# Optimization experiments

Measured on AMD Instinct MI355X. Metric: run time of the kernel, lower is better.

Reference implementation:

```python
import jax, jax.numpy as jnp
import numpy as np

N_NODES = 50000
N_EDGES = 800000
SIZES = [128, 256, 256, 128]
EPS = 1e-5


def setup_inputs() -> dict:
    key = jax.random.key(0)
    ks = jax.random.split(key, 2 + 5 * (len(SIZES) - 1))
    inp = {
        "x": jax.random.normal(ks[0], (N_NODES, SIZES[0]), dtype=jnp.float32),
        "edge_index": jax.random.randint(ks[1], (2, N_EDGES), 0, N_NODES, dtype=jnp.int64),
    }
    k = 2
    for i, (fin, fout) in enumerate(zip(SIZES[:-1], SIZES[1:])):
        scale = 1.0 / np.sqrt(fin)
        inp[f"W{i}"] = jax.random.normal(ks[k], (fout, fin), dtype=jnp.float32) * scale; k += 1
        inp[f"b{i}"] = jnp.zeros((fout,), dtype=jnp.float32)
        inp[f"g{i}"] = jnp.ones((fout,), dtype=jnp.float32)   # LayerNorm weight
        inp[f"be{i}"] = jnp.zeros((fout,), dtype=jnp.float32)  # LayerNorm bias
        inp[f"a{i}"] = jnp.full((1,), 0.25, dtype=jnp.float32)  # PReLU slope
        k += 3  # keep key consumption deterministic
    return inp


def _gcn_conv(x, src, dst, dinv, W, b):
    # GCNConv: h = x @ W^T; aggregate norm(src,dst) * h[src] into dst; add bias.
    h = x @ W.T  # [N, F_out]
    norm = dinv[src] * dinv[dst]  # [E+N]
    msg = norm[:, None] * h[src]  # [E+N, F_out]
    return jax.ops.segment_sum(msg, dst, num_segments=N_NODES) + b


def _layernorm_graph(x, g, be):
    # PyG LayerNorm(mode='graph'): normalize over all nodes and channels.
    mu = x.mean()
    xc = x - mu
    var = (xc * xc).mean()
    return xc / jnp.sqrt(var + EPS) * g + be


def _prelu(x, a):
    return jnp.where(x >= 0, x, a * x)


def reference(x, edge_index, W0, b0, g0, be0, a0, W1, b1, g1, be1, a1, W2, b2, g2, be2, a2):
    loop = jnp.arange(N_NODES, dtype=edge_index.dtype)
    src = jnp.concatenate([edge_index[0], loop])  # add self-loops
    dst = jnp.concatenate([edge_index[1], loop])
    deg = jax.ops.segment_sum(jnp.ones_like(dst, dtype=x.dtype), dst, num_segments=N_NODES)
    dinv = jax.lax.rsqrt(deg)  # deg >= 1 due to self-loops
    params = [(W0, b0, g0, be0, a0), (W1, b1, g1, be1, a1), (W2, b2, g2, be2, a2)]
    for W, b, g, be, a in params:
        x = _gcn_conv(x, src, dst, dinv, W, b)
        x = _layernorm_graph(x, g, be)
        x = _prelu(x, a)
    return x
```

## Files before the change

kernel.cpp:

```cpp
#include <hip/hip_runtime.h>

#define N_NODES 50000
#define N_EDGES 800000
#define EPS 1e-5f

typedef __attribute__((ext_vector_type(8))) short bf16x8;
typedef __attribute__((ext_vector_type(4))) float f32x4;
typedef __attribute__((ext_vector_type(4))) unsigned short us4;

__device__ __forceinline__ unsigned short f2b(float f) {
    union { float f; unsigned int u; } v; v.f = f;
    unsigned int r = v.u + 0x7fffu + ((v.u >> 16) & 1u);
    return (unsigned short)(r >> 16);
}
__device__ __forceinline__ float b2f(unsigned short b) {
    union { unsigned int u; float f; } v; v.u = ((unsigned int)b) << 16;
    return v.f;
}

#define RED_BUCKETS 64
#define RED_FLOATS_PER_LAYER (RED_BUCKETS * 16)


__global__ void init_kernel(int* __restrict__ deg, int* __restrict__ fill,
                            float* __restrict__ red, int n) {
    int i = blockIdx.x * blockDim.x + threadIdx.x;
    if (i < n) { deg[i] = 0; fill[i] = 0; }
    if (i < 3 * RED_FLOATS_PER_LAYER) red[i] = 0.f;
}

__global__ void count_kernel(const int* __restrict__ dst, int* __restrict__ deg, int e) {
    for (int i = blockIdx.x * blockDim.x + threadIdx.x; i < e; i += gridDim.x * blockDim.x)
        atomicAdd(&deg[dst[i]], 1);
}

__global__ void scan1_kernel(const int* __restrict__ deg, float* __restrict__ dinv,
                             int* __restrict__ bsum, int n) {
    int i = blockIdx.x * 256 + threadIdx.x;
    int v = (i < n) ? deg[i] : 0;
    if (i < n) dinv[i] = rsqrtf((float)(v + 1));
    int t = v;
    #pragma unroll
    for (int off = 1; off < 64; off <<= 1) t += __shfl_xor(t, off);
    __shared__ int wsum[4];
    int wid = threadIdx.x >> 6, lane = threadIdx.x & 63;
    if (lane == 0) wsum[wid] = t;
    __syncthreads();
    if (threadIdx.x == 0) bsum[blockIdx.x] = wsum[0] + wsum[1] + wsum[2] + wsum[3];
}

__global__ void scan2_kernel(const int* __restrict__ bsum, int* __restrict__ bpre, int nb) {
    __shared__ int sm[256];
    int t = threadIdx.x;
    sm[t] = (t < nb) ? bsum[t] : 0;
    __syncthreads();
    #pragma unroll
    for (int d = 1; d < 256; d <<= 1) {
        int x = (t >= d) ? sm[t - d] : 0;
        __syncthreads();
        sm[t] += x;
        __syncthreads();
    }
    bpre[t] = (t > 0) ? sm[t - 1] : 0;
}

__global__ void scan3_kernel(const int* __restrict__ deg, const int* __restrict__ bpre,
                             int* __restrict__ off, int n) {
    __shared__ int sm[256];
    int t = threadIdx.x;
    int i = blockIdx.x * 256 + t;
    int v = (i < n) ? deg[i] : 0;
    sm[t] = v;
    __syncthreads();
    #pragma unroll
    for (int d = 1; d < 256; d <<= 1) {
        int x = (t >= d) ? sm[t - d] : 0;
        __syncthreads();
        sm[t] += x;
        __syncthreads();
    }
    if (i < n) off[i + 1] = sm[t] + bpre[blockIdx.x];
    if (i == 0) off[0] = 0;
}

__global__ void scatter_kernel(const int* __restrict__ src, const int* __restrict__ dst,
                               const int* __restrict__ coff, int* __restrict__ fill,
                               const float* __restrict__ dinv,
                               int2* __restrict__ epack, int e) {
    for (int i = blockIdx.x * blockDim.x + threadIdx.x; i < e; i += gridDim.x * blockDim.x) {
        int d = dst[i];
        int s = src[i];
        int pos = coff[d] + atomicAdd(&fill[d], 1);
        epack[pos] = make_int2(s, __float_as_int(dinv[s] * dinv[d]));
    }
}


#define CV_NX (N_NODES * 128 / 4)
#define CV_N0 (256 * 128 / 4)
#define CV_N1 (256 * 256 / 4)
#define CV_N2 (128 * 256 / 4)

__global__ void convert_all(const float* __restrict__ x0, const float* __restrict__ W0,
                            const float* __restrict__ W1, const float* __restrict__ W2,
                            unsigned short* __restrict__ xb, unsigned short* __restrict__ wb0,
                            unsigned short* __restrict__ wb1, unsigned short* __restrict__ wb2) {
    int i = blockIdx.x * 256 + threadIdx.x;
    const float* s;
    unsigned short* d;
    int j = i;
    if (j < CV_NX) { s = x0; d = xb; }
    else if ((j -= CV_NX) < CV_N0) { s = W0; d = wb0; }
    else if ((j -= CV_N0) < CV_N1) { s = W1; d = wb1; }
    else if ((j -= CV_N1) < CV_N2) { s = W2; d = wb2; }
    else return;
    float4 v = reinterpret_cast<const float4*>(s)[j];
    us4 o;
    o[0] = f2b(v.x); o[1] = f2b(v.y); o[2] = f2b(v.z); o[3] = f2b(v.w);
    reinterpret_cast<us4*>(d)[j] = o;
}


template<int BN, bool TRANSFORM, bool ADD_BIAS, bool FUSE_RED>
__global__ __launch_bounds__(256) void gemm_fused(
    const unsigned short* __restrict__ Xin, const unsigned short* __restrict__ Wb,
    const float* __restrict__ bias, const float* __restrict__ redin,
    const float* __restrict__ gw, const float* __restrict__ bw,
    const float* __restrict__ asl, float* __restrict__ redout,
    unsigned short* __restrict__ Hout, int M, int K, float inv_count) {
    constexpr int FR_N = BN / 64;
    __shared__ unsigned short xs[64 * 32];
    __shared__ unsigned short wsm[BN * 32];
    int m0 = blockIdx.x * 64;
    int tid = threadIdx.x;
    int wid = tid >> 6, lane = tid & 63;
    int l16 = lane & 15, kg = lane >> 4;
    int srow = tid >> 2, sblk = tid & 3;

    float mu = 0.f, rstd = 0.f, alpha = 0.f;
    if (TRANSFORM) {
        float s = redin[lane * 16], s2 = redin[lane * 16 + 1];
        #pragma unroll
        for (int off = 1; off < 64; off <<= 1) { s += __shfl_xor(s, off); s2 += __shfl_xor(s2, off); }
        mu = s * inv_count;
        rstd = rsqrtf(s2 * inv_count - mu * mu + EPS);
        alpha = asl[0];
    }

    f32x4 acc[4][FR_N] = {};
    for (int k0 = 0; k0 < K; k0 += 32) {
        int gm = m0 + srow;
        bf16x8 xv = {};
        if (gm < M) {
            bf16x8 u = *reinterpret_cast<const bf16x8*>(Xin + (size_t)gm * K + k0 + sblk * 8);
            if (TRANSFORM) {
                #pragma unroll
                for (int i = 0; i < 8; ++i) {
                    int f = k0 + sblk * 8 + i;
                    float v = (b2f((unsigned short)u[i]) - mu) * rstd * gw[f] + bw[f];
                    v = v >= 0.f ? v : alpha * v;
                    xv[i] = (short)f2b(v);
                }
            } else {
                xv = u;
            }
        }
        *reinterpret_cast<bf16x8*>(xs + srow * 32 + ((sblk ^ (srow & 3)) * 8)) = xv;
        #pragma unroll
        for (int i = 0; i < BN / 64; ++i) {
            int idx = tid + i * 256;
            int wrow = idx >> 2, wblk = idx & 3;
            bf16x8 wv = *reinterpret_cast<const bf16x8*>(Wb + (size_t)wrow * K + k0 + wblk * 8);
            *reinterpret_cast<bf16x8*>(wsm + wrow * 32 + ((wblk ^ (wrow & 3)) * 8)) = wv;
        }
        __syncthreads();
        bf16x8 a[4], b[FR_N];
        #pragma unroll
        for (int f = 0; f < 4; ++f) {
            int ar = f * 16 + l16;
            a[f] = *reinterpret_cast<const bf16x8*>(xs + ar * 32 + ((kg ^ (ar & 3)) * 8));
        }
        #pragma unroll
        for (int f = 0; f < FR_N; ++f) {
            int br = wid * (FR_N * 16) + f * 16 + l16;
            b[f] = *reinterpret_cast<const bf16x8*>(wsm + br * 32 + ((kg ^ (br & 3)) * 8));
        }
        #pragma unroll
        for (int i = 0; i < 4; ++i)
            #pragma unroll
            for (int j = 0; j < FR_N; ++j)
                acc[i][j] = __builtin_amdgcn_mfma_f32_16x16x32_bf16(a[i], b[j], acc[i][j], 0, 0, 0);
        __syncthreads();
    }

    float s = 0.f, s2 = 0.f;
    #pragma unroll
    for (int i = 0; i < 4; ++i) {
        #pragma unroll
        for (int j = 0; j < FR_N; ++j) {
            int col = wid * (FR_N * 16) + j * 16 + l16;
            float bv = ADD_BIAS ? bias[col] : 0.f;
            #pragma unroll
            for (int r = 0; r < 4; ++r) {
                int row = m0 + i * 16 + kg * 4 + r;
                if (row < M) {
                    float v = acc[i][j][r] + bv;
                    if (FUSE_RED) { s += v; s2 += v * v; }
                    Hout[(size_t)row * BN + col] = f2b(v);
                }
            }
        }
    }
    if (FUSE_RED) {
        #pragma unroll
        for (int off = 1; off < 64; off <<= 1) { s += __shfl_xor(s, off); s2 += __shfl_xor(s2, off); }
        if (lane == 0) {
            int bkt = (blockIdx.x & (RED_BUCKETS - 1)) * 16;
            atomicAdd(&redout[bkt], s);
            atomicAdd(&redout[bkt + 1], s2);
        }
    }
}


template<int COLS, bool ADD_BIAS, bool FUSE_RED>
__global__ void aggregate2(const unsigned short* __restrict__ Hb,
                           const int* __restrict__ coff, const int2* __restrict__ epack,
                           const float* __restrict__ dinv,
                           const float* __restrict__ bias, unsigned short* __restrict__ Y,
                           float* __restrict__ red) {
    constexpr int RL = COLS / 8;
    constexpr int NG = 64 / RL;
    int node = blockIdx.x * 4 + (threadIdx.x >> 6);
    int lane = threadIdx.x & 63;
    int g = lane / RL;
    int rl = lane % RL;
    float di = dinv[node];
    int s0 = coff[node], s1 = coff[node + 1];
    float acc[8] = {};

    int k = s0 - 1 + g;
    int2 ec;
    bf16x8 vc;
    bool have = (k < s1);
    if (have) {
        if (k < s0) ec = make_int2(node, __float_as_int(di * di));
        else ec = epack[k];
        vc = *reinterpret_cast<const bf16x8*>(Hb + (size_t)ec.x * COLS + rl * 8);
    }
    while (have) {
        int k2 = k + NG;
        bool have2 = (k2 < s1);
        int2 en;
        bf16x8 vn;
        if (have2) {
            en = epack[k2];
            vn = *reinterpret_cast<const bf16x8*>(Hb + (size_t)en.x * COLS + rl * 8);
        }
        float w = __int_as_float(ec.y);
        #pragma unroll
        for (int i = 0; i < 8; ++i) acc[i] += w * b2f((unsigned short)vc[i]);
        k = k2; ec = en; vc = vn; have = have2;
    }

    #pragma unroll
    for (int off = RL; off < 64; off <<= 1) {
        #pragma unroll
        for (int i = 0; i < 8; ++i) acc[i] += __shfl_xor(acc[i], off);
    }
    if (ADD_BIAS) {
        #pragma unroll
        for (int i = 0; i < 8; ++i) acc[i] += bias[rl * 8 + i];
    }
    if (FUSE_RED) {
        float s = 0.f, s2 = 0.f;
        if (g == 0) {
            #pragma unroll
            for (int i = 0; i < 8; ++i) { s += acc[i]; s2 += acc[i] * acc[i]; }
        }
        #pragma unroll
        for (int off = 1; off < 64; off <<= 1) { s += __shfl_xor(s, off); s2 += __shfl_xor(s2, off); }
        if (lane == 0) {
            int bkt = (blockIdx.x & (RED_BUCKETS - 1)) * 16;
            atomicAdd(&red[bkt], s);
            atomicAdd(&red[bkt + 1], s2);
        }
    }
    if (g == 0) {
        bf16x8 o;
        #pragma unroll
        for (int i = 0; i < 8; ++i) o[i] = (short)f2b(acc[i]);
        __builtin_nontemporal_store(o, reinterpret_cast<bf16x8*>(Y + (size_t)node * COLS + rl * 8));
    }
}


__global__ void norm_final(const unsigned short* __restrict__ Yb, const float* __restrict__ red,
                           const float* __restrict__ g, const float* __restrict__ be,
                           const float* __restrict__ a, float* __restrict__ X,
                           int fmask8, int n8, float inv_count) {
    int lane = threadIdx.x & 63;
    float s = red[lane * 16], s2 = red[lane * 16 + 1];
    #pragma unroll
    for (int off = 1; off < 64; off <<= 1) { s += __shfl_xor(s, off); s2 += __shfl_xor(s2, off); }
    float mu = s * inv_count;
    float rstd = rsqrtf(s2 * inv_count - mu * mu + EPS);
    float alpha = a[0];
    for (int i = blockIdx.x * blockDim.x + threadIdx.x; i < n8; i += gridDim.x * blockDim.x) {
        bf16x8 v = reinterpret_cast<const bf16x8*>(Yb)[i];
        int fb = (i & fmask8) * 8;
        float o[8];
        #pragma unroll
        for (int j = 0; j < 8; ++j) {
            float t = (b2f((unsigned short)v[j]) - mu) * rstd * g[fb + j] + be[fb + j];
            o[j] = t >= 0.f ? t : alpha * t;
        }
        float* xp = X + (size_t)i * 8;
        *reinterpret_cast<float4*>(xp) = make_float4(o[0], o[1], o[2], o[3]);
        *reinterpret_cast<float4*>(xp + 4) = make_float4(o[4], o[5], o[6], o[7]);
    }
}


extern "C" void kernel_launch(void* const* d_in, const int* in_sizes, int n_in,
                              void* d_out, int out_size, void* d_ws, size_t ws_size,
                              hipStream_t stream) {
    const float* x0 = (const float*)d_in[0];
    const int* ei = (const int*)d_in[1];
    const float* W[3] = {(const float*)d_in[2], (const float*)d_in[7], (const float*)d_in[12]};
    const float* bb[3] = {(const float*)d_in[3], (const float*)d_in[8], (const float*)d_in[13]};
    const float* gg[3] = {(const float*)d_in[4], (const float*)d_in[9], (const float*)d_in[14]};
    const float* be[3] = {(const float*)d_in[5], (const float*)d_in[10], (const float*)d_in[15]};
    const float* aa[3] = {(const float*)d_in[6], (const float*)d_in[11], (const float*)d_in[16]};

    char* ws = (char*)d_ws;
    size_t o = 0;
    auto alloc = [&](size_t bytes) {
        void* p = ws + o;
        o = (o + bytes + 255) & ~(size_t)255;
        return p;
    };
    int* deg = (int*)alloc(N_NODES * 4);
    int* fill = (int*)alloc(N_NODES * 4);
    int* coff = (int*)alloc((N_NODES + 1) * 4);
    int2* epack = (int2*)alloc((size_t)N_EDGES * 8);
    float* dinv = (float*)alloc(N_NODES * 4);
    int* bsum = (int*)alloc(256 * 4);
    int* bpre = (int*)alloc(256 * 4);
    float* red = (float*)alloc(3 * RED_FLOATS_PER_LAYER * 4);
    unsigned short* Wb0 = (unsigned short*)alloc(256 * 128 * 2);
    unsigned short* Wb1 = (unsigned short*)alloc(256 * 256 * 2);
    unsigned short* Wb2 = (unsigned short*)alloc(128 * 256 * 2);
    unsigned short* xb = (unsigned short*)alloc((size_t)N_NODES * 128 * 2);
    unsigned short* hb = (unsigned short*)alloc((size_t)N_NODES * 256 * 2);
    unsigned short* yb = (unsigned short*)alloc((size_t)N_NODES * 256 * 2);

    const int* e_src = ei;
    const int* e_dst = ei + N_EDGES;
    int nb = (N_NODES + 255) / 256;

    init_kernel<<<(N_NODES + 255) / 256, 256, 0, stream>>>(deg, fill, red, N_NODES);
    count_kernel<<<2048, 256, 0, stream>>>(e_dst, deg, N_EDGES);
    scan1_kernel<<<nb, 256, 0, stream>>>(deg, dinv, bsum, N_NODES);
    scan2_kernel<<<1, 256, 0, stream>>>(bsum, bpre, nb);
    scan3_kernel<<<nb, 256, 0, stream>>>(deg, bpre, coff, N_NODES);
    scatter_kernel<<<2048, 256, 0, stream>>>(e_src, e_dst, coff, fill, dinv, epack, N_EDGES);

    int cvtot = CV_NX + CV_N0 + CV_N1 + CV_N2;
    convert_all<<<(cvtot + 255) / 256, 256, 0, stream>>>(x0, W[0], W[1], W[2], xb, Wb0, Wb1, Wb2);

    int gm = (N_NODES + 63) / 64;

    aggregate2<128, false, false><<<12500, 256, 0, stream>>>(xb, coff, epack, dinv,
                                                             nullptr, hb, nullptr);
    gemm_fused<256, false, true, true><<<gm, 256, 0, stream>>>(
        hb, Wb0, bb[0], nullptr, nullptr, nullptr, nullptr, red + 0, yb, N_NODES, 128,
        1.0f / (N_NODES * 256.0f));

    gemm_fused<256, true, false, false><<<gm, 256, 0, stream>>>(
        yb, Wb1, nullptr, red + 0, gg[0], be[0], aa[0], nullptr, hb, N_NODES, 256,
        1.0f / (N_NODES * 256.0f));
    aggregate2<256, true, true><<<12500, 256, 0, stream>>>(
        hb, coff, epack, dinv, bb[1], yb, red + RED_FLOATS_PER_LAYER);

    gemm_fused<128, true, false, false><<<gm, 256, 0, stream>>>(
        yb, Wb2, nullptr, red + RED_FLOATS_PER_LAYER, gg[1], be[1], aa[1], nullptr, hb,
        N_NODES, 256, 1.0f / (N_NODES * 256.0f));
    aggregate2<128, true, true><<<12500, 256, 0, stream>>>(
        hb, coff, epack, dinv, bb[2], yb, red + 2 * RED_FLOATS_PER_LAYER);

    norm_final<<<2048, 256, 0, stream>>>(yb, red + 2 * RED_FLOATS_PER_LAYER, gg[2], be[2], aa[2],
                                         (float*)d_out, 15, N_NODES * 128 / 8,
                                         1.0f / (N_NODES * 128.0f));
}
```

Measured before the change: 341.2 us.

## Pack edges into 32-bit words, double-buffer GEMM, and fold init into conversion

Each CSR edge is now one 32-bit word: a 16-bit source index plus a bf16 normalisation weight, where it used to be an int2. This halves edge traffic in the three aggregation passes. The GEMM stages only the activation tile in double-buffered LDS and reads weight fragments straight from global memory. It swaps the MFMA operand order so outputs go out as vectorised 4-element row stores, and folds LayerNorm/PReLU into fused fma form with vector loads of gamma/beta. Counter and reduction zeroing is merged into the conversion kernel to drop one launch. The risks are the bf16 precision loss on edge weights and a 16-bit index that only holds while there are fewer than 65536 nodes.

```diff
diff --git a/kernel.cpp b/kernel.cpp
--- a/kernel.cpp
+++ b/kernel.cpp
@@ -22,90 +22,20 @@
 #define RED_FLOATS_PER_LAYER (RED_BUCKETS * 16)
 
 
-__global__ void init_kernel(int* __restrict__ deg, int* __restrict__ fill,
-                            float* __restrict__ red, int n) {
-    int i = blockIdx.x * blockDim.x + threadIdx.x;
-    if (i < n) { deg[i] = 0; fill[i] = 0; }
-    if (i < 3 * RED_FLOATS_PER_LAYER) red[i] = 0.f;
-}
-
-__global__ void count_kernel(const int* __restrict__ dst, int* __restrict__ deg, int e) {
-    for (int i = blockIdx.x * blockDim.x + threadIdx.x; i < e; i += gridDim.x * blockDim.x)
-        atomicAdd(&deg[dst[i]], 1);
-}
-
-__global__ void scan1_kernel(const int* __restrict__ deg, float* __restrict__ dinv,
-                             int* __restrict__ bsum, int n) {
-    int i = blockIdx.x * 256 + threadIdx.x;
-    int v = (i < n) ? deg[i] : 0;
-    if (i < n) dinv[i] = rsqrtf((float)(v + 1));
-    int t = v;
-    #pragma unroll
-    for (int off = 1; off < 64; off <<= 1) t += __shfl_xor(t, off);
-    __shared__ int wsum[4];
-    int wid = threadIdx.x >> 6, lane = threadIdx.x & 63;
-    if (lane == 0) wsum[wid] = t;
-    __syncthreads();
-    if (threadIdx.x == 0) bsum[blockIdx.x] = wsum[0] + wsum[1] + wsum[2] + wsum[3];
-}
-
-__global__ void scan2_kernel(const int* __restrict__ bsum, int* __restrict__ bpre, int nb) {
-    __shared__ int sm[256];
-    int t = threadIdx.x;
-    sm[t] = (t < nb) ? bsum[t] : 0;
-    __syncthreads();
-    #pragma unroll
-    for (int d = 1; d < 256; d <<= 1) {
-        int x = (t >= d) ? sm[t - d] : 0;
-        __syncthreads();
-        sm[t] += x;
-        __syncthreads();
-    }
-    bpre[t] = (t > 0) ? sm[t - 1] : 0;
-}
-
-__global__ void scan3_kernel(const int* __restrict__ deg, const int* __restrict__ bpre,
-                             int* __restrict__ off, int n) {
-    __shared__ int sm[256];
-    int t = threadIdx.x;
-    int i = blockIdx.x * 256 + t;
-    int v = (i < n) ? deg[i] : 0;
-    sm[t] = v;
-    __syncthreads();
-    #pragma unroll
-    for (int d = 1; d < 256; d <<= 1) {
-        int x = (t >= d) ? sm[t - d] : 0;
-        __syncthreads();
-        sm[t] += x;
-        __syncthreads();
-    }
-    if (i < n) off[i + 1] = sm[t] + bpre[blockIdx.x];
-    if (i == 0) off[0] = 0;
-}
-
-__global__ void scatter_kernel(const int* __restrict__ src, const int* __restrict__ dst,
-                               const int* __restrict__ coff, int* __restrict__ fill,
-                               const float* __restrict__ dinv,
-                               int2* __restrict__ epack, int e) {
-    for (int i = blockIdx.x * blockDim.x + threadIdx.x; i < e; i += gridDim.x * blockDim.x) {
-        int d = dst[i];
-        int s = src[i];
-        int pos = coff[d] + atomicAdd(&fill[d], 1);
-        epack[pos] = make_int2(s, __float_as_int(dinv[s] * dinv[d]));
-    }
-}
-
-
 #define CV_NX (N_NODES * 128 / 4)
 #define CV_N0 (256 * 128 / 4)
 #define CV_N1 (256 * 256 / 4)
 #define CV_N2 (128 * 256 / 4)
 
-__global__ void convert_all(const float* __restrict__ x0, const float* __restrict__ W0,
+__global__ void prep_kernel(const float* __restrict__ x0, const float* __restrict__ W0,
                             const float* __restrict__ W1, const float* __restrict__ W2,
                             unsigned short* __restrict__ xb, unsigned short* __restrict__ wb0,
-                            unsigned short* __restrict__ wb1, unsigned short* __restrict__ wb2) {
+                            unsigned short* __restrict__ wb1, unsigned short* __restrict__ wb2,
+                            int* __restrict__ deg, int* __restrict__ fill,
+                            float* __restrict__ red) {
     int i = blockIdx.x * 256 + threadIdx.x;
+    if (i < N_NODES) { deg[i] = 0; fill[i] = 0; }
+    if (i < 3 * RED_FLOATS_PER_LAYER) red[i] = 0.f;
     const float* s;
     unsigned short* d;
     int j = i;
@@ -121,21 +51,88 @@
 }
 
 
+__global__ void count_kernel(const int* __restrict__ dst, int* __restrict__ deg, int e) {
+    for (int i = blockIdx.x * blockDim.x + threadIdx.x; i < e; i += gridDim.x * blockDim.x)
+        atomicAdd(&deg[dst[i]], 1);
+}
+
+__global__ void scan1_kernel(const int* __restrict__ deg, float* __restrict__ dinv,
+                             int* __restrict__ bsum, int n) {
+    int i = blockIdx.x * 256 + threadIdx.x;
+    int v = (i < n) ? deg[i] : 0;
+    if (i < n) dinv[i] = rsqrtf((float)(v + 1));
+    int t = v;
+    #pragma unroll
+    for (int off = 1; off < 64; off <<= 1) t += __shfl_xor(t, off);
+    __shared__ int wsum[4];
+    int wid = threadIdx.x >> 6, lane = threadIdx.x & 63;
+    if (lane == 0) wsum[wid] = t;
+    __syncthreads();
+    if (threadIdx.x == 0) bsum[blockIdx.x] = wsum[0] + wsum[1] + wsum[2] + wsum[3];
+}
+
+__global__ void scan2_kernel(const int* __restrict__ bsum, int* __restrict__ bpre, int nb) {
+    __shared__ int sm[256];
+    int t = threadIdx.x;
+    sm[t] = (t < nb) ? bsum[t] : 0;
+    __syncthreads();
+    #pragma unroll
+    for (int d = 1; d < 256; d <<= 1) {
+        int x = (t >= d) ? sm[t - d] : 0;
+        __syncthreads();
+        sm[t] += x;
+        __syncthreads();
+    }
+    bpre[t] = (t > 0) ? sm[t - 1] : 0;
+}
+
+__global__ void scan3_kernel(const int* __restrict__ deg, const int* __restrict__ bpre,
+                             int* __restrict__ off, int n) {
+    __shared__ int sm[256];
+    int t = threadIdx.x;
+    int i = blockIdx.x * 256 + t;
+    int v = (i < n) ? deg[i] : 0;
+    sm[t] = v;
+    __syncthreads();
+    #pragma unroll
+    for (int d = 1; d < 256; d <<= 1) {
+        int x = (t >= d) ? sm[t - d] : 0;
+        __syncthreads();
+        sm[t] += x;
+        __syncthreads();
+    }
+    if (i < n) off[i + 1] = sm[t] + bpre[blockIdx.x];
+    if (i == 0) off[0] = 0;
+}
+
+__global__ void scatter_kernel(const int* __restrict__ src, const int* __restrict__ dst,
+                               const int* __restrict__ coff, int* __restrict__ fill,
+                               const float* __restrict__ dinv,
+                               unsigned int* __restrict__ epack, int e) {
+    for (int i = blockIdx.x * blockDim.x + threadIdx.x; i < e; i += gridDim.x * blockDim.x) {
+        int d = dst[i];
+        int s = src[i];
+        int pos = coff[d] + atomicAdd(&fill[d], 1);
+        epack[pos] = ((unsigned int)f2b(dinv[s] * dinv[d]) << 16) | (unsigned int)s;
+    }
+}
+
+
 template<int BN, bool TRANSFORM, bool ADD_BIAS, bool FUSE_RED>
-__global__ __launch_bounds__(256) void gemm_fused(
+__device__ __forceinline__ void gemm_body(
     const unsigned short* __restrict__ Xin, const unsigned short* __restrict__ Wb,
     const float* __restrict__ bias, const float* __restrict__ redin,
     const float* __restrict__ gw, const float* __restrict__ bw,
     const float* __restrict__ asl, float* __restrict__ redout,
     unsigned short* __restrict__ Hout, int M, int K, float inv_count) {
     constexpr int FR_N = BN / 64;
-    __shared__ unsigned short xs[64 * 32];
-    __shared__ unsigned short wsm[BN * 32];
-    int m0 = blockIdx.x * 64;
+    __shared__ unsigned short xs[2][64 * 32];
     int tid = threadIdx.x;
     int wid = tid >> 6, lane = tid & 63;
     int l16 = lane & 15, kg = lane >> 4;
     int srow = tid >> 2, sblk = tid & 3;
+    int m0 = blockIdx.x * 64;
+    int colbase = wid * (BN / 4);
 
     float mu = 0.f, rstd = 0.f, alpha = 0.f;
     if (TRANSFORM) {
@@ -147,67 +144,85 @@
         alpha = asl[0];
     }
 
-    f32x4 acc[4][FR_N] = {};
-    for (int k0 = 0; k0 < K; k0 += 32) {
-        int gm = m0 + srow;
+    int gm = m0 + srow;
+    bool inm = (gm < M);
+    const unsigned short* xrow = Xin + (size_t)gm * K + sblk * 8;
+    unsigned short* xdst = &xs[0][srow * 32 + ((sblk ^ (srow & 3)) * 8)];
+
+    auto stage = [&](int k0, int buf) {
         bf16x8 xv = {};
-        if (gm < M) {
-            bf16x8 u = *reinterpret_cast<const bf16x8*>(Xin + (size_t)gm * K + k0 + sblk * 8);
+        if (inm) {
+            bf16x8 u = *reinterpret_cast<const bf16x8*>(xrow + k0);
             if (TRANSFORM) {
+                int f0 = k0 + sblk * 8;
+                float ga[8], ba[8];
+                *reinterpret_cast<float4*>(&ga[0]) = *reinterpret_cast<const float4*>(gw + f0);
+                *reinterpret_cast<float4*>(&ga[4]) = *reinterpret_cast<const float4*>(gw + f0 + 4);
+                *reinterpret_cast<float4*>(&ba[0]) = *reinterpret_cast<const float4*>(bw + f0);
+                *reinterpret_cast<float4*>(&ba[4]) = *reinterpret_cast<const float4*>(bw + f0 + 4);
                 #pragma unroll
                 for (int i = 0; i < 8; ++i) {
-                    int f = k0 + sblk * 8 + i;
-                    float v = (b2f((unsigned short)u[i]) - mu) * rstd * gw[f] + bw[f];
-                    v = v >= 0.f ? v : alpha * v;
+                    float A = rstd * ga[i];
+                    float B = ba[i] - mu * A;
+                    float v = fmaf(b2f((unsigned short)u[i]), A, B);
+                    v = fmaf(fminf(v, 0.f), alpha - 1.0f, v);
                     xv[i] = (short)f2b(v);
                 }
             } else {
                 xv = u;
             }
         }
-        *reinterpret_cast<bf16x8*>(xs + srow * 32 + ((sblk ^ (srow & 3)) * 8)) = xv;
-        #pragma unroll
-        for (int i = 0; i < BN / 64; ++i) {
-            int idx = tid + i * 256;
-            int wrow = idx >> 2, wblk = idx & 3;
-            bf16x8 wv = *reinterpret_cast<const bf16x8*>(Wb + (size_t)wrow * K + k0 + wblk * 8);
-            *reinterpret_cast<bf16x8*>(wsm + wrow * 32 + ((wblk ^ (wrow & 3)) * 8)) = wv;
-        }
+        *reinterpret_cast<bf16x8*>(xdst + buf * (64 * 32)) = xv;
+    };
+
+    stage(0, 0);
+    f32x4 acc[4][FR_N] = {};
+    int nsteps = K / 32;
+    for (int s = 0; s < nsteps; ++s) {
         __syncthreads();
-        bf16x8 a[4], b[FR_N];
-        #pragma unroll
-        for (int f = 0; f < 4; ++f) {
-            int ar = f * 16 + l16;
-            a[f] = *reinterpret_cast<const bf16x8*>(xs + ar * 32 + ((kg ^ (ar & 3)) * 8));
-        }
-        #pragma unroll
-        for (int f = 0; f < FR_N; ++f) {
-            int br = wid * (FR_N * 16) + f * 16 + l16;
-            b[f] = *reinterpret_cast<const bf16x8*>(wsm + br * 32 + ((kg ^ (br & 3)) * 8));
+        int k0 = s * 32;
+        if (s + 1 < nsteps) stage(k0 + 32, (s + 1) & 1);
+        bf16x8 b[FR_N];
+        #pragma unroll
+        for (int j = 0; j < FR_N; ++j)
+            b[j] = *reinterpret_cast<const bf16x8*>(
+                Wb + (size_t)(colbase + j * 16 + l16) * K + k0 + kg * 8);
+        const unsigned short* xbuf = xs[s & 1];
+        bf16x8 a[4];
+        #pragma unroll
+        for (int i = 0; i < 4; ++i) {
+            int ar = i * 16 + l16;
+            a[i] = *reinterpret_cast<const bf16x8*>(xbuf + ar * 32 + ((kg ^ (ar & 3)) * 8));
         }
         #pragma unroll
         for (int i = 0; i < 4; ++i)
             #pragma unroll
             for (int j = 0; j < FR_N; ++j)
-                acc[i][j] = __builtin_amdgcn_mfma_f32_16x16x32_bf16(a[i], b[j], acc[i][j], 0, 0, 0);
-        __syncthreads();
-    }
-
+                acc[i][j] = __builtin_amdgcn_mfma_f32_16x16x32_bf16(b[j], a[i], acc[i][j], 0, 0, 0);
+    }
+
+    float bsel[FR_N][4];
+    if (ADD_BIAS) {
+        #pragma unroll
+        for (int j = 0; j < FR_N; ++j)
+            *reinterpret_cast<float4*>(bsel[j]) =
+                *reinterpret_cast<const float4*>(bias + colbase + j * 16 + kg * 4);
+    }
     float s = 0.f, s2 = 0.f;
     #pragma unroll
     for (int i = 0; i < 4; ++i) {
-        #pragma unroll
-        for (int j = 0; j < FR_N; ++j) {
-            int col = wid * (FR_N * 16) + j * 16 + l16;
-            float bv = ADD_BIAS ? bias[col] : 0.f;
+        int row = m0 + i * 16 + l16;
+        if (row < M) {
             #pragma unroll
-            for (int r = 0; r < 4; ++r) {
-                int row = m0 + i * 16 + kg * 4 + r;
-                if (row < M) {
-                    float v = acc[i][j][r] + bv;
+            for (int j = 0; j < FR_N; ++j) {
+                us4 o;
+                #pragma unroll
+                for (int r = 0; r < 4; ++r) {
+                    float v = acc[i][j][r] + (ADD_BIAS ? bsel[j][r] : 0.f);
                     if (FUSE_RED) { s += v; s2 += v * v; }
-                    Hout[(size_t)row * BN + col] = f2b(v);
+                    o[r] = f2b(v);
                 }
+                *reinterpret_cast<us4*>(Hout + (size_t)row * BN + colbase + j * 16 + kg * 4) = o;
             }
         }
     }
@@ -224,11 +239,11 @@
 
 
 template<int COLS, bool ADD_BIAS, bool FUSE_RED>
-__global__ void aggregate2(const unsigned short* __restrict__ Hb,
-                           const int* __restrict__ coff, const int2* __restrict__ epack,
-                           const float* __restrict__ dinv,
-                           const float* __restrict__ bias, unsigned short* __restrict__ Y,
-                           float* __restrict__ red) {
+__device__ __forceinline__ void agg_body(
+    const unsigned short* __restrict__ Hb, const int* __restrict__ coff,
+    const unsigned int* __restrict__ epack, const float* __restrict__ dinv,
+    const float* __restrict__ bias, unsigned short* __restrict__ Y,
+    float* __restrict__ red) {
     constexpr int RL = COLS / 8;
     constexpr int NG = 64 / RL;
     int node = blockIdx.x * 4 + (threadIdx.x >> 6);
@@ -240,27 +255,27 @@
     float acc[8] = {};
 
     int k = s0 - 1 + g;
-    int2 ec;
+    int sc; float wc;
     bf16x8 vc;
     bool have = (k < s1);
     if (have) {
-        if (k < s0) ec = make_int2(node, __float_as_int(di * di));
-        else ec = epack[k];
-        vc = *reinterpret_cast<const bf16x8*>(Hb + (size_t)ec.x * COLS + rl * 8);
+        if (k < s0) { sc = node; wc = di * di; }
+        else { unsigned int u = epack[k]; sc = u & 0xffff; wc = b2f((unsigned short)(u >> 16)); }
+        vc = *reinterpret_cast<const bf16x8*>(Hb + (size_t)sc * COLS + rl * 8);
     }
     while (have) {
         int k2 = k + NG;
         bool have2 = (k2 < s1);
-        int2 en;
+        int sn = 0; float wn = 0.f;
         bf16x8 vn;
         if (have2) {
-            en = epack[k2];
-            vn = *reinterpret_cast<const bf16x8*>(Hb + (size_t)en.x * COLS + rl * 8);
-        }
-        float w = __int_as_float(ec.y);
-        #pragma unroll
-        for (int i = 0; i < 8; ++i) acc[i] += w * b2f((unsigned short)vc[i]);
-        k = k2; ec = en; vc = vn; have = have2;
+            unsigned int u = epack[k2];
+            sn = u & 0xffff; wn = b2f((unsigned short)(u >> 16));
+            vn = *reinterpret_cast<const bf16x8*>(Hb + (size_t)sn * COLS + rl * 8);
+        }
+        #pragma unroll
+        for (int i = 0; i < 8; ++i) acc[i] += wc * b2f((unsigned short)vc[i]);
+        k = k2; wc = wn; vc = vn; have = have2;
     }
 
     #pragma unroll
@@ -292,6 +307,35 @@
         for (int i = 0; i < 8; ++i) o[i] = (short)f2b(acc[i]);
         __builtin_nontemporal_store(o, reinterpret_cast<bf16x8*>(Y + (size_t)node * COLS + rl * 8));
     }
+}
+
+
+__global__ __launch_bounds__(256) void gemm_l0(const unsigned short* X, const unsigned short* W,
+                                               const float* bias, float* redout,
+                                               unsigned short* H, int M, int K, float ic) {
+    gemm_body<256, false, true, true>(X, W, bias, nullptr, nullptr, nullptr, nullptr, redout, H, M, K, ic);
+}
+__global__ __launch_bounds__(256) void gemm_l1(const unsigned short* X, const unsigned short* W,
+                                               const float* redin, const float* gw, const float* bw,
+                                               const float* asl, unsigned short* H, int M, int K, float ic) {
+    gemm_body<256, true, false, false>(X, W, nullptr, redin, gw, bw, asl, nullptr, H, M, K, ic);
+}
+__global__ __launch_bounds__(256) void gemm_l2(const unsigned short* X, const unsigned short* W,
+                                               const float* redin, const float* gw, const float* bw,
+                                               const float* asl, unsigned short* H, int M, int K, float ic) {
+    gemm_body<128, true, false, false>(X, W, nullptr, redin, gw, bw, asl, nullptr, H, M, K, ic);
+}
+__global__ void agg_l0(const unsigned short* Hb, const int* coff, const unsigned int* ep,
+                       const float* dinv, unsigned short* Y) {
+    agg_body<128, false, false>(Hb, coff, ep, dinv, nullptr, Y, nullptr);
+}
+__global__ void agg_l1(const unsigned short* Hb, const int* coff, const unsigned int* ep,
+                       const float* dinv, const float* bias, unsigned short* Y, float* red) {
+    agg_body<256, true, true>(Hb, coff, ep, dinv, bias, Y, red);
+}
+__global__ void agg_l2(const unsigned short* Hb, const int* coff, const unsigned int* ep,
+                       const float* dinv, const float* bias, unsigned short* Y, float* red) {
+    agg_body<128, true, true>(Hb, coff, ep, dinv, bias, Y, red);
 }
 
 
@@ -343,7 +387,7 @@
     int* deg = (int*)alloc(N_NODES * 4);
     int* fill = (int*)alloc(N_NODES * 4);
     int* coff = (int*)alloc((N_NODES + 1) * 4);
-    int2* epack = (int2*)alloc((size_t)N_EDGES * 8);
+    unsigned int* epack = (unsigned int*)alloc((size_t)N_EDGES * 4);
     float* dinv = (float*)alloc(N_NODES * 4);
     int* bsum = (int*)alloc(256 * 4);
     int* bpre = (int*)alloc(256 * 4);
@@ -359,37 +403,30 @@
     const int* e_dst = ei + N_EDGES;
     int nb = (N_NODES + 255) / 256;
 
-    init_kernel<<<(N_NODES + 255) / 256, 256, 0, stream>>>(deg, fill, red, N_NODES);
+    int cvtot = CV_NX + CV_N0 + CV_N1 + CV_N2;
+    prep_kernel<<<(cvtot + 255) / 256, 256, 0, stream>>>(x0, W[0], W[1], W[2], xb, Wb0, Wb1, Wb2,
+                                                         deg, fill, red);
     count_kernel<<<2048, 256, 0, stream>>>(e_dst, deg, N_EDGES);
     scan1_kernel<<<nb, 256, 0, stream>>>(deg, dinv, bsum, N_NODES);
     scan2_kernel<<<1, 256, 0, stream>>>(bsum, bpre, nb);
     scan3_kernel<<<nb, 256, 0, stream>>>(deg, bpre, coff, N_NODES);
     scatter_kernel<<<2048, 256, 0, stream>>>(e_src, e_dst, coff, fill, dinv, epack, N_EDGES);
 
-    int cvtot = CV_NX + CV_N0 + CV_N1 + CV_N2;
-    convert_all<<<(cvtot + 255) / 256, 256, 0, stream>>>(x0, W[0], W[1], W[2], xb, Wb0, Wb1, Wb2);
-
     int gm = (N_NODES + 63) / 64;
-
-    aggregate2<128, false, false><<<12500, 256, 0, stream>>>(xb, coff, epack, dinv,
-                                                             nullptr, hb, nullptr);
-    gemm_fused<256, false, true, true><<<gm, 256, 0, stream>>>(
-        hb, Wb0, bb[0], nullptr, nullptr, nullptr, nullptr, red + 0, yb, N_NODES, 128,
-        1.0f / (N_NODES * 256.0f));
-
-    gemm_fused<256, true, false, false><<<gm, 256, 0, stream>>>(
-        yb, Wb1, nullptr, red + 0, gg[0], be[0], aa[0], nullptr, hb, N_NODES, 256,
-        1.0f / (N_NODES * 256.0f));
-    aggregate2<256, true, true><<<12500, 256, 0, stream>>>(
-        hb, coff, epack, dinv, bb[1], yb, red + RED_FLOATS_PER_LAYER);
-
-    gemm_fused<128, true, false, false><<<gm, 256, 0, stream>>>(
-        yb, Wb2, nullptr, red + RED_FLOATS_PER_LAYER, gg[1], be[1], aa[1], nullptr, hb,
-        N_NODES, 256, 1.0f / (N_NODES * 256.0f));
-    aggregate2<128, true, true><<<12500, 256, 0, stream>>>(
-        hb, coff, epack, dinv, bb[2], yb, red + 2 * RED_FLOATS_PER_LAYER);
+    float ic256 = 1.0f / (N_NODES * 256.0f);
+    float ic128 = 1.0f / (N_NODES * 128.0f);
+
+    agg_l0<<<12500, 256, 0, stream>>>(xb, coff, epack, dinv, hb);
+    gemm_l0<<<gm, 256, 0, stream>>>(hb, Wb0, bb[0], red + 0, yb, N_NODES, 128, ic256);
+
+    gemm_l1<<<gm, 256, 0, stream>>>(yb, Wb1, red + 0, gg[0], be[0], aa[0], hb, N_NODES, 256, ic256);
+    agg_l1<<<12500, 256, 0, stream>>>(hb, coff, epack, dinv, bb[1], yb, red + RED_FLOATS_PER_LAYER);
+
+    gemm_l2<<<gm, 256, 0, stream>>>(yb, Wb2, red + RED_FLOATS_PER_LAYER, gg[1], be[1], aa[1], hb,
+                                    N_NODES, 256, ic256);
+    agg_l2<<<12500, 256, 0, stream>>>(hb, coff, epack, dinv, bb[2], yb,
+                                      red + 2 * RED_FLOATS_PER_LAYER);
 
     norm_final<<<2048, 256, 0, stream>>>(yb, red + 2 * RED_FLOATS_PER_LAYER, gg[2], be[2], aa[2],
-                                         (float*)d_out, 15, N_NODES * 128 / 8,
-                                         1.0f / (N_NODES * 128.0f));
-}
+                                         (float*)d_out, 15, N_NODES * 128 / 8, ic128);
+}
```

Measured after the change: 341.1 us. Within noise of the previous version (-0.0%).
